# Kernel optimization log

Hardware: AMD Instinct MI355X
Metric: run time of the kernel (lower is better)

## Reference

```python
import jax, jax.numpy as jnp
import numpy as np

INPUT, HIDDEN, OUTPUT = 512, 1024, 512
BATCH, SEQ = 128, 256


def setup_inputs() -> dict:
    key = jax.random.key(0)
    ks = jax.random.split(key, 14)
    s_in = 1.0 / np.sqrt(INPUT)
    s_h = 1.0 / np.sqrt(HIDDEN)
    d = {
        "x_seq": jax.random.normal(ks[0], (BATCH, SEQ, INPUT), jnp.float32),
        "Wxf_w": jax.random.uniform(ks[1], (HIDDEN, INPUT), jnp.float32, -s_in, s_in),
        "Wxf_b": jax.random.uniform(ks[2], (HIDDEN,), jnp.float32, -s_in, s_in),
        "Whf_w": jax.random.uniform(ks[3], (HIDDEN, HIDDEN), jnp.float32, -s_h, s_h),
        "Wxi_w": jax.random.uniform(ks[4], (HIDDEN, INPUT), jnp.float32, -s_in, s_in),
        "Wxi_b": jax.random.uniform(ks[5], (HIDDEN,), jnp.float32, -s_in, s_in),
        "Whi_w": jax.random.uniform(ks[6], (HIDDEN, HIDDEN), jnp.float32, -s_h, s_h),
        "Wxg_w": jax.random.uniform(ks[7], (HIDDEN, INPUT), jnp.float32, -s_in, s_in),
        "Wxg_b": jax.random.uniform(ks[8], (HIDDEN,), jnp.float32, -s_in, s_in),
        "Whg_w": jax.random.uniform(ks[9], (HIDDEN, HIDDEN), jnp.float32, -s_h, s_h),
        "Wxo_w": jax.random.uniform(ks[10], (HIDDEN, INPUT), jnp.float32, -s_in, s_in),
        "Wxo_b": jax.random.uniform(ks[11], (HIDDEN,), jnp.float32, -s_in, s_in),
        "Who_w": jax.random.uniform(ks[12], (HIDDEN, HIDDEN), jnp.float32, -s_h, s_h),
        "Why_w": jax.random.uniform(ks[13], (OUTPUT, HIDDEN), jnp.float32, -s_h, s_h),
        "Why_b": jnp.zeros((OUTPUT,), jnp.float32),
    }
    return d


def _lstm(x_seq, Wxf_w, Wxf_b, Whf_w, Wxi_w, Wxi_b, Whi_w,
          Wxg_w, Wxg_b, Whg_w, Wxo_w, Wxo_b, Who_w, Why_w, Why_b):
    batch, seq_len, _ = x_seq.shape
    hidden = Whf_w.shape[0]
    # Precompute input projections for all timesteps (one big GEMM per gate).
    xf = jnp.einsum('bsi,hi->bsh', x_seq, Wxf_w) + Wxf_b  # (B,S,H)
    xi = jnp.einsum('bsi,hi->bsh', x_seq, Wxi_w) + Wxi_b
    xg = jnp.einsum('bsi,hi->bsh', x_seq, Wxg_w) + Wxg_b
    xo = jnp.einsum('bsi,hi->bsh', x_seq, Wxo_w) + Wxo_b
    # time-major for scan: (S, B, H)
    xs = jnp.stack([xf, xi, xg, xo], axis=0).transpose(2, 0, 1, 3)  # (S,4,B,H)

    h0 = jnp.zeros((batch, hidden), x_seq.dtype)
    c0 = jnp.zeros((batch, hidden), x_seq.dtype)

    def step(carry, x_t):
        h, c = carry
        xf_t, xi_t, xg_t, xo_t = x_t[0], x_t[1], x_t[2], x_t[3]
        f_t = jax.nn.sigmoid(xf_t + h @ Whf_w.T)
        i_t = jax.nn.sigmoid(xi_t + h @ Whi_w.T)
        g_t = jnp.tanh(xg_t + h @ Whg_w.T)
        c = f_t * c + i_t * g_t
        o_t = jax.nn.sigmoid(xo_t + h @ Who_w.T)
        h = o_t * jnp.tanh(c)
        return (h, c), None

    (h, c), _ = jax.lax.scan(step, (h0, c0), xs)
    out = h @ Why_w.T + Why_b
    return out, h, c


def reference(x_seq, Wxf_w, Wxf_b, Whf_w, Wxi_w, Wxi_b, Whi_w,
              Wxg_w, Wxg_b, Whg_w, Wxo_w, Wxo_b, Who_w, Why_w, Why_b):
    return _lstm(x_seq, Wxf_w, Wxf_b, Whf_w, Wxi_w, Wxi_b, Whi_w,
                 Wxg_w, Wxg_b, Whg_w, Wxo_w, Wxo_b, Who_w, Why_w, Why_b)
```

## Files before the change

kernel.cpp:

```cpp
#include <hip/hip_runtime.h>


#define B_ 128
#define S_ 256
#define I_ 512
#define H_ 1024
#define O_ 512

typedef unsigned short u16;
typedef unsigned int u32;
typedef unsigned long long u64;

typedef short v8s __attribute__((ext_vector_type(8)));
typedef unsigned int v4u __attribute__((ext_vector_type(4)));
typedef float v16f __attribute__((ext_vector_type(16)));
typedef float v4f __attribute__((ext_vector_type(4)));

__device__ __forceinline__ u16 f2bf(float f) {
  u32 u = __float_as_uint(f);
  u32 r = (u + 0x7fffu + ((u >> 16) & 1u)) >> 16;
  return (u16)r;
}
__device__ __forceinline__ u32 pack2(float a, float b) {
  return (u32)f2bf(a) | ((u32)f2bf(b) << 16);
}
__device__ __forceinline__ uint4 cvt8(const float* __restrict__ s) {
  float4 f0 = ((const float4*)s)[0];
  float4 f1 = ((const float4*)s)[1];
  uint4 o;
  o.x = pack2(f0.x, f0.y); o.y = pack2(f0.z, f0.w);
  o.z = pack2(f1.x, f1.y); o.w = pack2(f1.z, f1.w);
  return o;
}

__device__ __forceinline__ uint4 uc_ld16(const u16* p) {
  u64 lo = __hip_atomic_load((const u64*)p, __ATOMIC_RELAXED, __HIP_MEMORY_SCOPE_AGENT);
  u64 hi = __hip_atomic_load((const u64*)p + 1, __ATOMIC_RELAXED, __HIP_MEMORY_SCOPE_AGENT);
  uint4 v; v.x = (u32)lo; v.y = (u32)(lo >> 32); v.z = (u32)hi; v.w = (u32)(hi >> 32);
  return v;
}
__device__ __forceinline__ void uc_st16(u16* p, uint4 v) {
  v4u d;
  d.x = v.x; d.y = v.y; d.z = v.z; d.w = v.w;
  asm volatile("global_store_dwordx4 %0, %1, off sc0 sc1"
               :: "v"(p), "v"(d) : "memory");
}

__global__ void lstm_prep(
    const float* __restrict__ x,
    const float* __restrict__ Whf, const float* __restrict__ Whi,
    const float* __restrict__ Whg, const float* __restrict__ Who,
    const float* __restrict__ Wxf, const float* __restrict__ Wxi,
    const float* __restrict__ Wxg, const float* __restrict__ Wxo,
    const float* __restrict__ bfp, const float* __restrict__ bip,
    const float* __restrict__ bgp, const float* __restrict__ bop,
    const float* __restrict__ Why,
    u16* __restrict__ xt, u16* __restrict__ Wc, float* __restrict__ bc,
    u16* __restrict__ WhyT, u16* __restrict__ hbuf, u32* __restrict__ barrier)
{
  const int gid = blockIdx.x * blockDim.x + threadIdx.x;
  const int gsz = gridDim.x * blockDim.x;

  if (gid < 256) barrier[gid] = 0u;

  for (int v = gid; v < (S_ * B_ * I_ / 8); v += gsz) {
    int flat = v * 8;
    int b = flat / (S_ * I_);
    int rem = flat - b * (S_ * I_);
    int t = rem / I_;
    int i = rem - t * I_;
    size_t dst = ((size_t)(t * 4 + (b >> 5)) * 64 + (i >> 3)) * 32 + (b & 31);
    ((uint4*)xt)[dst] = cvt8(x + flat);
  }

  for (int o = gid; o < 192 * 4096; o += gsz) {
    int w8 = o >> 12;
    int colG = o & 4095;
    int unit = ((colG >> 6) << 4) + (((colG >> 5) & 1) << 3) + ((colG >> 2) & 7);
    int g = colG & 3;
    const float* Whp = (g == 0) ? Whf : (g == 1) ? Whi : (g == 2) ? Whg : Who;
    const float* Wxp = (g == 0) ? Wxf : (g == 1) ? Wxi : (g == 2) ? Wxg : Wxo;
    const float* s = (w8 < 64) ? (Wxp + (size_t)unit * 512 + w8 * 8)
                               : (Whp + (size_t)unit * 1024 + (w8 - 64) * 8);
    ((uint4*)Wc)[o] = cvt8(s);
  }

  for (int n = gid; n < 4096; n += gsz) {
    int unit = ((n >> 6) << 4) + (((n >> 5) & 1) << 3) + ((n >> 2) & 7);
    int g = n & 3;
    const float* bp = (g == 0) ? bfp : (g == 1) ? bip : (g == 2) ? bgp : bop;
    bc[n] = bp[unit];
  }

  for (int v = gid; v < (O_ * H_ / 8); v += gsz) {
    int flat = v * 8;
    *(uint4*)(WhyT + flat) = cvt8(Why + flat);
  }

  for (int v = gid; v < 2 * 16384; v += gsz) {
    uint4 z; z.x = 0; z.y = 0; z.z = 0; z.w = 0;
    ((uint4*)hbuf)[v] = z;
  }
}

__global__ __launch_bounds__(256, 1) void lstm_seq(
    const u16* __restrict__ xt, const u16* __restrict__ Wc,
    const float* __restrict__ bc, u16* __restrict__ hbuf,
    const u16* __restrict__ WhyT, const float* __restrict__ WhyB,
    float* __restrict__ out, u32* __restrict__ barrier, int rotFlag)
{
  __shared__ float scr[2048];
  __shared__ u16 hstage[512];

  const int tid  = threadIdx.x;
  const int lane = tid & 63;
  const int w    = tid >> 6;
  const int ct   = w & 1;
  const int kh   = w >> 1;
  const int rq   = blockIdx.x >> 6;
  const int cg   = blockIdx.x & 63;
  const bool rot = (rotFlag != 0);

  const int colN  = lane & 31;
  const int kgsel = lane >> 5;
  const int colG  = cg * 64 + ct * 32 + colN;
  const int gate  = colN & 3;
  const int unitL = ct * 8 + (colN >> 2);
  const float bias = bc[colG];

  const uint4* xA4  = (const uint4*)xt;
  const uint4* WcF4 = (const uint4*)Wc;
  uint4*       HA4  = (uint4*)hbuf;

  const int xaOff = rq * 2048 + kh * 1024 + lane;
  const int xbOff = kh * 131072 + kgsel * 4096 + colG;
  const int haOff = rq * 4096 + kh * 2048 + lane;
  const int hbOff = 262144 + kh * 262144 + kgsel * 4096 + colG;

  float c[8];
#pragma unroll
  for (int i = 0; i < 8; ++i) c[i] = 0.f;

  __builtin_amdgcn_fence(__ATOMIC_ACQUIRE, "agent");
  __syncthreads();

  v8s Bx[16], Bh[32];
  {
    const uint4* bx = WcF4 + xbOff;
#pragma unroll
    for (int kb = 0; kb < 16; ++kb)
      Bx[kb] = __builtin_bit_cast(v8s, bx[(size_t)kb * 8192]);
    const uint4* bh = WcF4 + hbOff;
#pragma unroll
    for (int kb = 0; kb < 32; ++kb)
      Bh[kb] = __builtin_bit_cast(v8s, bh[(size_t)kb * 8192]);
  }

  v16f acc0, acc1;

#pragma unroll 1
  for (int t = 0; t < S_; ++t) {
    const size_t tb = rot ? (size_t)t * 16384 : (size_t)(t & 1) * 16384;
    const size_t tn = rot ? (size_t)(t + 1) * 16384 : (size_t)((t & 1) ^ 1) * 16384;

#pragma unroll
    for (int i = 0; i < 16; ++i) { acc0[i] = 0.f; acc1[i] = 0.f; }

    {
      const uint4* ax = xA4 + (size_t)t * 8192 + xaOff;
      v8s xr[16];
#pragma unroll
      for (int kb = 0; kb < 16; ++kb)
        xr[kb] = __builtin_bit_cast(v8s, ax[kb * 64]);
#pragma unroll
      for (int kb = 0; kb < 16; ++kb) {
        if (kb & 1) acc1 = __builtin_amdgcn_mfma_f32_32x32x16_bf16(xr[kb], Bx[kb], acc1, 0, 0, 0);
        else        acc0 = __builtin_amdgcn_mfma_f32_32x32x16_bf16(xr[kb], Bx[kb], acc0, 0, 0, 0);
      }
    }

    if (t > 0) {
      if (tid == 0) {
        u32 spins = 0;
        while (__hip_atomic_load(&barrier[rq * 64], __ATOMIC_RELAXED,
                                 __HIP_MEMORY_SCOPE_AGENT) < 64u * (u32)t) {
          __builtin_amdgcn_s_sleep(1);
          if (++spins > (1u << 22)) break;
        }
      }
      __syncthreads();
    }

    {
      const uint4* ah = HA4 + tb + haOff;
      v8s hr[32];
      if (rot) {
#pragma unroll
        for (int kb = 0; kb < 32; ++kb)
          hr[kb] = __builtin_bit_cast(v8s, ah[kb * 64]);
      } else {
#pragma unroll
        for (int kb = 0; kb < 32; ++kb)
          hr[kb] = __builtin_bit_cast(v8s, uc_ld16((const u16*)(ah + kb * 64)));
      }
#pragma unroll
      for (int kb = 0; kb < 32; ++kb) {
        if (kb & 1) acc1 = __builtin_amdgcn_mfma_f32_32x32x16_bf16(hr[kb], Bh[kb], acc1, 0, 0, 0);
        else        acc0 = __builtin_amdgcn_mfma_f32_32x32x16_bf16(hr[kb], Bh[kb], acc0, 0, 0, 0);
      }
    }

    float aT[16];
#pragma unroll
    for (int i = 0; i < 16; ++i) aT[i] = acc0[i] + acc1[i];
    {
      int h2 = 1 - kh;
#pragma unroll
      for (int i = 0; i < 8; ++i)
        scr[ct * 1024 + h2 * 512 + i * 64 + lane] = aT[h2 * 8 + i];
    }
    __syncthreads();

    const bool lastT = (t == S_ - 1);
#pragma unroll
    for (int i = 0; i < 8; ++i) {
      int r = kh * 8 + i;
      float pre = aT[r] + scr[ct * 1024 + kh * 512 + i * 64 + lane] + bias;
      float e = __expf((gate == 2) ? (2.f * pre) : (-pre));
      float act = (gate == 2) ? (1.f - 2.f / (e + 1.f)) : (1.f / (1.f + e));
      int qb = lane & ~3;
      float F = __shfl(act, qb + 0, 64);
      float I = __shfl(act, qb + 1, 64);
      float G = __shfl(act, qb + 2, 64);
      float O = __shfl(act, qb + 3, 64);
      float cn = fmaf(F, c[i], I * G);
      c[i] = cn;
      float e2 = __expf(2.f * cn);
      float hv = O * (1.f - 2.f / (e2 + 1.f));
      if (gate == 0) {
        int rowL = (r & 3) + ((r >> 2) << 3) + (kgsel << 2);
        hstage[rowL * 16 + unitL] = f2bf(hv);
        if (lastT) {
          int grow = rq * 32 + rowL;
          int gunit = cg * 16 + unitL;
          out[65536 + grow * H_ + gunit] = hv;
          out[196608 + grow * H_ + gunit] = cn;
        }
      }
    }
    __syncthreads();

    if (tid < 64) {
      int row = tid >> 1, u16sel = tid & 1;
      uint4 v = ((const uint4*)hstage)[tid];
      uc_st16((u16*)(HA4 + tn + rq * 4096 + (size_t)(2 * cg + u16sel) * 32 + row), v);
      asm volatile("s_waitcnt vmcnt(0)" ::: "memory");
      if (tid == 0)
        atomicAdd(&barrier[rq * 64], 1u);
    }
  }

  {
    if (tid < 4) {
      u32 spins = 0;
      while (__hip_atomic_load(&barrier[tid * 64], __ATOMIC_RELAXED,
                               __HIP_MEMORY_SCOPE_AGENT) < 64u * (u32)S_) {
        __builtin_amdgcn_s_sleep(2);
        if (++spins > (1u << 22)) break;
      }
    }
  }
  __syncthreads();

  if (blockIdx.x < 32) {
    const int wg = blockIdx.x;
    const uint4* HF = HA4 + (rot ? (size_t)S_ * 16384 : 0);
    const int l15 = lane & 15;
    const int l4 = lane >> 4;
    const int colO = (wg << 4) + l15;
    v4f o0, o1;
#pragma unroll
    for (int i = 0; i < 4; ++i) { o0[i] = 0.f; o1[i] = 0.f; }
#pragma unroll 4
    for (int kc = 0; kc < 32; ++kc) {
      v8s bfrag = *(const v8s*)(WhyT + (size_t)colO * H_ + kc * 32 + (l4 << 3));
      size_t i0 = (size_t)w * 4096 + kc * 128 + l4 * 32 + l15;
      v8s a0, a1;
      if (rot) {
        a0 = __builtin_bit_cast(v8s, HF[i0]);
        a1 = __builtin_bit_cast(v8s, HF[i0 + 16]);
      } else {
        a0 = __builtin_bit_cast(v8s, uc_ld16((const u16*)(HF + i0)));
        a1 = __builtin_bit_cast(v8s, uc_ld16((const u16*)(HF + i0 + 16)));
      }
      o0 = __builtin_amdgcn_mfma_f32_16x16x32_bf16(a0, bfrag, o0, 0, 0, 0);
      o1 = __builtin_amdgcn_mfma_f32_16x16x32_bf16(a1, bfrag, o1, 0, 0, 0);
    }
    float bO = WhyB[colO];
#pragma unroll
    for (int r2 = 0; r2 < 4; ++r2) {
      int row = (w << 5) + (l4 << 2) + r2;
      out[row * O_ + colO] = o0[r2] + bO;
      out[(row + 16) * O_ + colO] = o1[r2] + bO;
    }
  }
}

extern "C" void kernel_launch(void* const* d_in, const int* in_sizes, int n_in,
                              void* d_out, int out_size, void* d_ws, size_t ws_size,
                              hipStream_t stream) {
  const float* x    = (const float*)d_in[0];
  const float* Wxf  = (const float*)d_in[1];
  const float* bf_  = (const float*)d_in[2];
  const float* Whf  = (const float*)d_in[3];
  const float* Wxi  = (const float*)d_in[4];
  const float* bi_  = (const float*)d_in[5];
  const float* Whi  = (const float*)d_in[6];
  const float* Wxg  = (const float*)d_in[7];
  const float* bg_  = (const float*)d_in[8];
  const float* Whg  = (const float*)d_in[9];
  const float* Wxo  = (const float*)d_in[10];
  const float* bo_  = (const float*)d_in[11];
  const float* Who  = (const float*)d_in[12];
  const float* Why  = (const float*)d_in[13];
  const float* Whyb = (const float*)d_in[14];

  char* ws = (char*)d_ws;
  u16*   xtp  = (u16*)(ws);
  u16*   Wcp  = (u16*)(ws + 33554432);
  float* bcp  = (float*)(ws + 46137344);
  u16*   WhyT = (u16*)(ws + 46153728);
  u32*   barp = (u32*)(ws + 47202304);
  u16*   hbuf = (u16*)(ws + 47203328);
  float* outp = (float*)d_out;

  const size_t need_rot = 47203328ull + 257ull * 262144ull;
  int rot = (ws_size >= need_rot) ? 1 : 0;

  lstm_prep<<<dim3(1024), dim3(256), 0, stream>>>(
      x, Whf, Whi, Whg, Who, Wxf, Wxi, Wxg, Wxo,
      bf_, bi_, bg_, bo_, Why, xtp, Wcp, bcp, WhyT, hbuf, barp);

  lstm_seq<<<dim3(256), dim3(256), 0, stream>>>(
      xtp, Wcp, bcp, hbuf, WhyT, Whyb, outp, barp, rot);
}
```

Baseline: 2.036 ms.

## Replace atomic counter barrier with data-as-flag polling on hidden-state buffer

When the rotating per-timestep h buffer is available, the atomic counter barrier is dropped. Consumers instead poll the h values with uncached loads until every element is nonzero. The bf16 conversion maps zero to the smallest denormal so that zero can act as a 'not yet written' sentinel, and the prep kernel clears all 257 slots (slot 0 filled with a nonzero h0). This removes the atomic add, spin-on-counter and syncthreads round trip from the critical path, but changes numerics slightly, adds a large zeroing pass, and relies on each 16-byte store being observed atomically.

```diff
diff --git a/kernel.cpp b/kernel.cpp
--- a/kernel.cpp
+++ b/kernel.cpp
@@ -19,6 +19,7 @@
 __device__ __forceinline__ u16 f2bf(float f) {
   u32 u = __float_as_uint(f);
   u32 r = (u + 0x7fffu + ((u >> 16) & 1u)) >> 16;
+  r += (r == 0u);
   return (u16)r;
 }
 __device__ __forceinline__ u32 pack2(float a, float b) {
@@ -56,7 +57,8 @@
     const float* __restrict__ bgp, const float* __restrict__ bop,
     const float* __restrict__ Why,
     u16* __restrict__ xt, u16* __restrict__ Wc, float* __restrict__ bc,
-    u16* __restrict__ WhyT, u16* __restrict__ hbuf, u32* __restrict__ barrier)
+    u16* __restrict__ WhyT, u16* __restrict__ hbuf, u32* __restrict__ barrier,
+    int rotFlag)
 {
   const int gid = blockIdx.x * blockDim.x + threadIdx.x;
   const int gsz = gridDim.x * blockDim.x;
@@ -97,9 +99,17 @@
     *(uint4*)(WhyT + flat) = cvt8(Why + flat);
   }
 
-  for (int v = gid; v < 2 * 16384; v += gsz) {
-    uint4 z; z.x = 0; z.y = 0; z.z = 0; z.w = 0;
-    ((uint4*)hbuf)[v] = z;
+  if (rotFlag) {
+    for (int v = gid; v < 257 * 16384; v += gsz) {
+      u32 wv = (v < 16384) ? 0x00010001u : 0u;
+      uint4 z; z.x = wv; z.y = wv; z.z = wv; z.w = wv;
+      ((uint4*)hbuf)[v] = z;
+    }
+  } else {
+    for (int v = gid; v < 2 * 16384; v += gsz) {
+      uint4 z; z.x = 0; z.y = 0; z.z = 0; z.w = 0;
+      ((uint4*)hbuf)[v] = z;
+    }
   }
 }
 
@@ -179,35 +189,60 @@
       }
     }
 
-    if (t > 0) {
-      if (tid == 0) {
-        u32 spins = 0;
-        while (__hip_atomic_load(&barrier[rq * 64], __ATOMIC_RELAXED,
-                                 __HIP_MEMORY_SCOPE_AGENT) < 64u * (u32)t) {
-          __builtin_amdgcn_s_sleep(1);
-          if (++spins > (1u << 22)) break;
+    v8s hr[32];
+    if (rot) {
+      const uint4* ah = HA4 + tb + haOff;
+      v4u t0[32];
+#pragma unroll
+      for (int kb = 0; kb < 32; ++kb)
+        asm volatile("global_load_dwordx4 %0, %1, off sc0 sc1"
+                     : "=v"(t0[kb]) : "v"((const u16*)(ah + kb * 64)) : "memory");
+      asm volatile("s_waitcnt vmcnt(0)" ::: "memory");
+      __builtin_amdgcn_sched_barrier(0);
+      u32 need = 0xffffffffu;
+      u32 spins = 0;
+      for (;;) {
+#pragma unroll
+        for (int kb = 0; kb < 32; ++kb)
+          if ((need >> kb) & 1u) {
+            int ok = (t0[kb].x != 0u) & (t0[kb].y != 0u) &
+                     (t0[kb].z != 0u) & (t0[kb].w != 0u);
+            if (__all(ok)) need &= ~(1u << kb);
+          }
+        if (!need || ++spins > (1u << 20)) break;
+#pragma unroll
+        for (int kb = 0; kb < 32; ++kb)
+          if ((need >> kb) & 1u)
+            asm volatile("global_load_dwordx4 %0, %1, off sc0 sc1"
+                         : "=v"(t0[kb]) : "v"((const u16*)(ah + kb * 64)) : "memory");
+        asm volatile("s_waitcnt vmcnt(0)" ::: "memory");
+        __builtin_amdgcn_sched_barrier(0);
+      }
+#pragma unroll
+      for (int kb = 0; kb < 32; ++kb)
+        hr[kb] = __builtin_bit_cast(v8s, t0[kb]);
+    } else {
+      if (t > 0) {
+        if (tid == 0) {
+          u32 spins = 0;
+          while (__hip_atomic_load(&barrier[rq * 64], __ATOMIC_RELAXED,
+                                   __HIP_MEMORY_SCOPE_AGENT) < 64u * (u32)t) {
+            __builtin_amdgcn_s_sleep(1);
+            if (++spins > (1u << 22)) break;
+          }
         }
-      }
-      __syncthreads();
-    }
-
-    {
+        __syncthreads();
+      }
       const uint4* ah = HA4 + tb + haOff;
-      v8s hr[32];
-      if (rot) {
-#pragma unroll
-        for (int kb = 0; kb < 32; ++kb)
-          hr[kb] = __builtin_bit_cast(v8s, ah[kb * 64]);
-      } else {
-#pragma unroll
-        for (int kb = 0; kb < 32; ++kb)
-          hr[kb] = __builtin_bit_cast(v8s, uc_ld16((const u16*)(ah + kb * 64)));
-      }
-#pragma unroll
-      for (int kb = 0; kb < 32; ++kb) {
-        if (kb & 1) acc1 = __builtin_amdgcn_mfma_f32_32x32x16_bf16(hr[kb], Bh[kb], acc1, 0, 0, 0);
-        else        acc0 = __builtin_amdgcn_mfma_f32_32x32x16_bf16(hr[kb], Bh[kb], acc0, 0, 0, 0);
-      }
+#pragma unroll
+      for (int kb = 0; kb < 32; ++kb)
+        hr[kb] = __builtin_bit_cast(v8s, uc_ld16((const u16*)(ah + kb * 64)));
+    }
+
+#pragma unroll
+    for (int kb = 0; kb < 32; ++kb) {
+      if (kb & 1) acc1 = __builtin_amdgcn_mfma_f32_32x32x16_bf16(hr[kb], Bh[kb], acc1, 0, 0, 0);
+      else        acc0 = __builtin_amdgcn_mfma_f32_32x32x16_bf16(hr[kb], Bh[kb], acc0, 0, 0, 0);
     }
 
     float aT[16];
@@ -254,13 +289,15 @@
       int row = tid >> 1, u16sel = tid & 1;
       uint4 v = ((const uint4*)hstage)[tid];
       uc_st16((u16*)(HA4 + tn + rq * 4096 + (size_t)(2 * cg + u16sel) * 32 + row), v);
-      asm volatile("s_waitcnt vmcnt(0)" ::: "memory");
-      if (tid == 0)
-        atomicAdd(&barrier[rq * 64], 1u);
-    }
-  }
-
-  {
+      if (!rot) {
+        asm volatile("s_waitcnt vmcnt(0)" ::: "memory");
+        if (tid == 0)
+          atomicAdd(&barrier[rq * 64], 1u);
+      }
+    }
+  }
+
+  if (!rot) {
     if (tid < 4) {
       u32 spins = 0;
       while (__hip_atomic_load(&barrier[tid * 64], __ATOMIC_RELAXED,
@@ -269,8 +306,8 @@
         if (++spins > (1u << 22)) break;
       }
     }
-  }
-  __syncthreads();
+    __syncthreads();
+  }
 
   if (blockIdx.x < 32) {
     const int wg = blockIdx.x;
@@ -281,14 +318,28 @@
     v4f o0, o1;
 #pragma unroll
     for (int i = 0; i < 4; ++i) { o0[i] = 0.f; o1[i] = 0.f; }
-#pragma unroll 4
+#pragma unroll 1
     for (int kc = 0; kc < 32; ++kc) {
       v8s bfrag = *(const v8s*)(WhyT + (size_t)colO * H_ + kc * 32 + (l4 << 3));
       size_t i0 = (size_t)w * 4096 + kc * 128 + l4 * 32 + l15;
       v8s a0, a1;
       if (rot) {
-        a0 = __builtin_bit_cast(v8s, HF[i0]);
-        a1 = __builtin_bit_cast(v8s, HF[i0 + 16]);
+        v4u A0, A1;
+        u32 spins = 0;
+        for (;;) {
+          asm volatile("global_load_dwordx4 %0, %1, off sc0 sc1"
+                       : "=v"(A0) : "v"((const u16*)(HF + i0)) : "memory");
+          asm volatile("global_load_dwordx4 %0, %1, off sc0 sc1"
+                       : "=v"(A1) : "v"((const u16*)(HF + i0 + 16)) : "memory");
+          asm volatile("s_waitcnt vmcnt(0)" ::: "memory");
+          __builtin_amdgcn_sched_barrier(0);
+          int ok = (A0.x != 0u) & (A0.y != 0u) & (A0.z != 0u) & (A0.w != 0u) &
+                   (A1.x != 0u) & (A1.y != 0u) & (A1.z != 0u) & (A1.w != 0u);
+          if (__all(ok) || ++spins > (1u << 20)) break;
+          __builtin_amdgcn_s_sleep(1);
+        }
+        a0 = __builtin_bit_cast(v8s, A0);
+        a1 = __builtin_bit_cast(v8s, A1);
       } else {
         a0 = __builtin_bit_cast(v8s, uc_ld16((const u16*)(HF + i0)));
         a1 = __builtin_bit_cast(v8s, uc_ld16((const u16*)(HF + i0 + 16)));
@@ -339,7 +390,7 @@
 
   lstm_prep<<<dim3(1024), dim3(256), 0, stream>>>(
       x, Whf, Whi, Whg, Who, Wxf, Wxi, Wxg, Wxo,
-      bf_, bi_, bg_, bo_, Why, xtp, Wcp, bcp, WhyT, hbuf, barp);
+      bf_, bi_, bg_, bo_, Why, xtp, Wcp, bcp, WhyT, hbuf, barp, rot);
 
   lstm_seq<<<dim3(256), dim3(256), 0, stream>>>(
       xtp, Wcp, bcp, hbuf, WhyT, Whyb, outp, barp, rot);
```

Result: slower. 2.473 ms (+21.4%).
